# Kernel optimization log

Measured on AMD Instinct MI355X. Metric: run time of the kernel, lower is better.

The kernel has to match this reference:

```python
import jax, jax.numpy as jnp
import numpy as np

B, IN_F, OUT_F, KD = 256, 1024, 128, 16


def setup_inputs() -> dict:
    key = jax.random.key(0)
    k1, k2 = jax.random.split(key)
    x = jax.random.normal(k1, (B, IN_F), dtype=jnp.float32)
    t_mat = jax.random.normal(k2, (IN_F, OUT_F, KD), dtype=jnp.float32)
    return {"x": x, "t_mat": t_mat}


def reference(x, t_mat):
    # Projection: [B, in] @ [in, out*kd] -> [B, out, kd]
    m = jnp.einsum('bi,iok->bok', x, t_mat)
    # All-pairs L1 distance over kernel dim: [B, B, out]
    norm = jnp.sum(jnp.abs(m[:, None, :, :] - m[None, :, :, :]), axis=-1)
    # exp(-norm) summed over the partner axis; subtract 1 for self-pair (norm=0 -> exp=1)
    o_b = jnp.sum(jnp.exp(-norm), axis=1) - 1.0  # [B, out]
    return jnp.concatenate([x, o_b], axis=1)  # [B, in + out]
```

## Files before the change

### kernel.cpp

```cpp
#include <hip/hip_runtime.h>
#include <hip/hip_fp16.h>


#define BATCH 256
#define INF   1024
#define OUTF  128
#define KDIM  16
#define TCOLS 2048
#define OCOLS 1152
#define XB    1032
#define PMW   12

typedef __attribute__((ext_vector_type(8))) short short8;
typedef __attribute__((ext_vector_type(4))) float f32x4;

__device__ inline unsigned pack_bf2(float lo, float hi) {
    return __builtin_amdgcn_perm(__float_as_uint(hi), __float_as_uint(lo), 0x07060302u);
}
__device__ inline unsigned short bf_trunc(float f) {
    return (unsigned short)(__float_as_uint(f) >> 16);
}

__global__ __launch_bounds__(512) void k_prep(const float* __restrict__ x,
                                              unsigned short* __restrict__ xf,
                                              float* __restrict__ out) {
    const int t = blockIdx.x * 512 + threadIdx.x;
    const int mt = t >> 11, ks = (t >> 6) & 31, lane = t & 63;
    const int l15 = lane & 15, q = lane >> 4;

    const float* src = x + (mt * 16 + l15) * INF + ks * 32 + q * 8;
    float4 v0 = *reinterpret_cast<const float4*>(src);
    float4 v1 = *reinterpret_cast<const float4*>(src + 4);
    union { unsigned u[4]; short8 s; } ua;
    ua.u[0] = pack_bf2(v0.x, v0.y);
    ua.u[1] = pack_bf2(v0.z, v0.w);
    ua.u[2] = pack_bf2(v1.x, v1.y);
    ua.u[3] = pack_bf2(v1.z, v1.w);
    reinterpret_cast<short8*>(xf)[t] = ua.s;

    #pragma unroll
    for (int j = t; j < 65536; j += 32768) {
        const int r = j >> 8, c = j & 255;
        reinterpret_cast<float4*>(out)[r * 288 + c] =
            reinterpret_cast<const float4*>(x)[j];
    }
}

__global__ __launch_bounds__(256, 2) void k_gemm(const float* __restrict__ T,
                                                 const unsigned short* __restrict__ xf,
                                                 __half* __restrict__ mh) {
    const int blk = blockIdx.x;
    const int o   = blk & 127;
    const int mq  = blk >> 7;
    const int tid = threadIdx.x;
    const int wave = tid >> 6, lane = tid & 63;
    const int l15 = lane & 15, q = lane >> 4;

    __shared__ unsigned short bs[16][XB];
    __shared__ __half pmout[64][16];

    const int mt = mq * 4 + wave;
    const short8* xr = reinterpret_cast<const short8*>(xf) + mt * 2048 + lane;

    short8 a[32];
    #pragma unroll
    for (int ks = 0; ks < 32; ++ks) a[ks] = xr[ks * 64];
    __builtin_amdgcn_sched_barrier(0);

    {
        const int kb = tid >> 2, n0 = (tid & 3) * 4;
        #pragma unroll
        for (int g = 0; g < 4; ++g) {
            float4 tv[4];
            #pragma unroll
            for (int p = 0; p < 4; ++p)
                tv[p] = *reinterpret_cast<const float4*>(
                    &T[((g * 4 + p) * 64 + kb) * TCOLS + o * KDIM + n0]);
            #pragma unroll
            for (int p = 0; p < 4; ++p) {
                const int k = (g * 4 + p) * 64 + kb;
                bs[n0 + 0][k] = bf_trunc(tv[p].x);
                bs[n0 + 1][k] = bf_trunc(tv[p].y);
                bs[n0 + 2][k] = bf_trunc(tv[p].z);
                bs[n0 + 3][k] = bf_trunc(tv[p].w);
            }
        }
    }
    __syncthreads();

    f32x4 acc = {0.f, 0.f, 0.f, 0.f};
    #pragma unroll
    for (int ks = 0; ks < 32; ++ks) {
        short8 bfr = *reinterpret_cast<const short8*>(&bs[l15][ks * 32 + q * 8]);
        acc = __builtin_amdgcn_mfma_f32_16x16x32_bf16(a[ks], bfr, acc, 0, 0, 0);
    }

    #pragma unroll
    for (int r = 0; r < 4; ++r)
        pmout[wave * 16 + q * 4 + r][l15] = __float2half(acc[r]);
    __syncthreads();

    if (tid < 128) {
        const int row = tid >> 1, hh = tid & 1;
        uint4 v = *reinterpret_cast<const uint4*>(&pmout[row][hh * 8]);
        *reinterpret_cast<uint4*>(&mh[o * (BATCH * KDIM) + (mq * 64 + row) * KDIM + hh * 8]) = v;
    }
}

__global__ __launch_bounds__(1024, 4) void k_pair(const __half* __restrict__ mh,
                                                  float* __restrict__ out) {
    const int blk = blockIdx.x;
    const int o   = blk & 127;
    const int h   = blk >> 7;
    const int tid = threadIdx.x;

    __shared__ __half2 pm[BATCH][PMW];
    __shared__ float part[32][128];

    if (tid < 512) {
        uint4 v = *reinterpret_cast<const uint4*>(
            &mh[o * (BATCH * KDIM) + (tid >> 1) * KDIM + (tid & 1) * 8]);
        *reinterpret_cast<uint4*>(&pm[tid >> 1][(tid & 1) * 4]) = v;
    }
    __syncthreads();

    const int i1 = tid & 31;
    const int bsel = tid >> 5;
    __half2 my[4][8];
    #pragma unroll
    for (int r = 0; r < 4; ++r) {
        union { uint4 u[2]; __half2 hh[8]; } c;
        c.u[0] = *reinterpret_cast<const uint4*>(&pm[h * 128 + r * 32 + i1][0]);
        c.u[1] = *reinterpret_cast<const uint4*>(&pm[h * 128 + r * 32 + i1][4]);
        #pragma unroll
        for (int j = 0; j < 8; ++j) my[r][j] = c.hh[j];
    }

    union U16 { uint4 u[2]; __half2 hh[8]; };
    float tot[4] = {0.f, 0.f, 0.f, 0.f};
    const int b2_lo = bsel * 8;

    U16 c0, c1;
    c0.u[0] = *reinterpret_cast<const uint4*>(&pm[b2_lo][0]);
    c0.u[1] = *reinterpret_cast<const uint4*>(&pm[b2_lo][4]);

    #pragma unroll
    for (int ib = 0; ib < 8; ib += 2) {
        c1.u[0] = *reinterpret_cast<const uint4*>(&pm[b2_lo + ib + 1][0]);
        c1.u[1] = *reinterpret_cast<const uint4*>(&pm[b2_lo + ib + 1][4]);
        #pragma unroll
        for (int r = 0; r < 4; ++r) {
            __half2 e0 = __habs2(__hsub2(my[r][0], c0.hh[0]));
            __half2 e1 = __habs2(__hsub2(my[r][1], c0.hh[1]));
            __half2 e2 = __habs2(__hsub2(my[r][2], c0.hh[2]));
            __half2 e3 = __habs2(__hsub2(my[r][3], c0.hh[3]));
            e0 = __hadd2(e0, __habs2(__hsub2(my[r][4], c0.hh[4])));
            e1 = __hadd2(e1, __habs2(__hsub2(my[r][5], c0.hh[5])));
            e2 = __hadd2(e2, __habs2(__hsub2(my[r][6], c0.hh[6])));
            e3 = __hadd2(e3, __habs2(__hsub2(my[r][7], c0.hh[7])));
            __half2 es = __hadd2(__hadd2(e0, e1), __hadd2(e2, e3));
            float n = __low2float(es) + __high2float(es);
            tot[r] += __expf(-n);
        }
        if (ib + 2 < 8) {
            c0.u[0] = *reinterpret_cast<const uint4*>(&pm[b2_lo + ib + 2][0]);
            c0.u[1] = *reinterpret_cast<const uint4*>(&pm[b2_lo + ib + 2][4]);
        }
        #pragma unroll
        for (int r = 0; r < 4; ++r) {
            __half2 e0 = __habs2(__hsub2(my[r][0], c1.hh[0]));
            __half2 e1 = __habs2(__hsub2(my[r][1], c1.hh[1]));
            __half2 e2 = __habs2(__hsub2(my[r][2], c1.hh[2]));
            __half2 e3 = __habs2(__hsub2(my[r][3], c1.hh[3]));
            e0 = __hadd2(e0, __habs2(__hsub2(my[r][4], c1.hh[4])));
            e1 = __hadd2(e1, __habs2(__hsub2(my[r][5], c1.hh[5])));
            e2 = __hadd2(e2, __habs2(__hsub2(my[r][6], c1.hh[6])));
            e3 = __hadd2(e3, __habs2(__hsub2(my[r][7], c1.hh[7])));
            __half2 es = __hadd2(__hadd2(e0, e1), __hadd2(e2, e3));
            float n = __low2float(es) + __high2float(es);
            tot[r] += __expf(-n);
        }
    }
    #pragma unroll
    for (int r = 0; r < 4; ++r)
        part[bsel][r * 32 + i1] = tot[r];
    __syncthreads();

    {
        const int g = tid >> 7, b1 = tid & 127;
        float s = part[g * 4 + 0][b1] + part[g * 4 + 1][b1]
                + part[g * 4 + 2][b1] + part[g * 4 + 3][b1];
        __syncthreads();
        part[g * 4][b1] = s;
    }
    __syncthreads();
    if (tid < 128) {
        float s = -1.0f;
        #pragma unroll
        for (int g = 0; g < 8; ++g) s += part[g * 4][tid];
        out[(h * 128 + tid) * OCOLS + INF + o] = s;
    }
}

extern "C" void kernel_launch(void* const* d_in, const int* in_sizes, int n_in,
                              void* d_out, int out_size, void* d_ws, size_t ws_size,
                              hipStream_t stream) {
    const float* x = (const float*)d_in[0];
    const float* T = (const float*)d_in[1];
    float* out = (float*)d_out;
    unsigned short* xf = (unsigned short*)d_ws;
    __half* mh = (__half*)((char*)d_ws + (1u << 20));

    k_prep<<<64, 512, 0, stream>>>(x, xf, out);
    k_gemm<<<512, 256, 0, stream>>>(T, xf, mh);
    k_pair<<<256, 1024, 0, stream>>>(mh, out);
}
```

Baseline: 80.02 us.

## Fuse projection GEMM into pairwise kernel, removing intermediate global buffer

Merges the bf16 MFMA projection kernel into the pairwise L1/exp kernel. Each 1024-thread block computes the full 256x16 projection for its output feature directly into shared memory, which removes one launch and the global round trip through the fp16 intermediate. Both blocks with the same output feature (h=0,1) now recompute the same projection, doubling GEMM work and T reads. Register use is kept down by double-buffering A fragments in groups of 8.

```diff
diff --git a/kernel.cpp b/kernel.cpp
--- a/kernel.cpp
+++ b/kernel.cpp
@@ -46,81 +46,79 @@
     }
 }
 
-__global__ __launch_bounds__(256, 2) void k_gemm(const float* __restrict__ T,
-                                                 const unsigned short* __restrict__ xf,
-                                                 __half* __restrict__ mh) {
-    const int blk = blockIdx.x;
-    const int o   = blk & 127;
-    const int mq  = blk >> 7;
-    const int tid = threadIdx.x;
-    const int wave = tid >> 6, lane = tid & 63;
-    const int l15 = lane & 15, q = lane >> 4;
-
-    __shared__ unsigned short bs[16][XB];
-    __shared__ __half pmout[64][16];
-
-    const int mt = mq * 4 + wave;
-    const short8* xr = reinterpret_cast<const short8*>(xf) + mt * 2048 + lane;
-
-    short8 a[32];
-    #pragma unroll
-    for (int ks = 0; ks < 32; ++ks) a[ks] = xr[ks * 64];
-    __builtin_amdgcn_sched_barrier(0);
-
-    {
-        const int kb = tid >> 2, n0 = (tid & 3) * 4;
-        #pragma unroll
-        for (int g = 0; g < 4; ++g) {
-            float4 tv[4];
-            #pragma unroll
-            for (int p = 0; p < 4; ++p)
-                tv[p] = *reinterpret_cast<const float4*>(
-                    &T[((g * 4 + p) * 64 + kb) * TCOLS + o * KDIM + n0]);
-            #pragma unroll
-            for (int p = 0; p < 4; ++p) {
-                const int k = (g * 4 + p) * 64 + kb;
-                bs[n0 + 0][k] = bf_trunc(tv[p].x);
-                bs[n0 + 1][k] = bf_trunc(tv[p].y);
-                bs[n0 + 2][k] = bf_trunc(tv[p].z);
-                bs[n0 + 3][k] = bf_trunc(tv[p].w);
-            }
-        }
-    }
-    __syncthreads();
-
-    f32x4 acc = {0.f, 0.f, 0.f, 0.f};
-    #pragma unroll
-    for (int ks = 0; ks < 32; ++ks) {
-        short8 bfr = *reinterpret_cast<const short8*>(&bs[l15][ks * 32 + q * 8]);
-        acc = __builtin_amdgcn_mfma_f32_16x16x32_bf16(a[ks], bfr, acc, 0, 0, 0);
-    }
-
-    #pragma unroll
-    for (int r = 0; r < 4; ++r)
-        pmout[wave * 16 + q * 4 + r][l15] = __float2half(acc[r]);
-    __syncthreads();
-
-    if (tid < 128) {
-        const int row = tid >> 1, hh = tid & 1;
-        uint4 v = *reinterpret_cast<const uint4*>(&pmout[row][hh * 8]);
-        *reinterpret_cast<uint4*>(&mh[o * (BATCH * KDIM) + (mq * 64 + row) * KDIM + hh * 8]) = v;
-    }
-}
-
-__global__ __launch_bounds__(1024, 4) void k_pair(const __half* __restrict__ mh,
-                                                  float* __restrict__ out) {
+__global__ __launch_bounds__(1024, 4) void k_fused2(const float* __restrict__ T,
+                                                    const unsigned short* __restrict__ xf,
+                                                    float* __restrict__ out) {
     const int blk = blockIdx.x;
     const int o   = blk & 127;
     const int h   = blk >> 7;
     const int tid = threadIdx.x;
-
+    const int wave = tid >> 6, lane = tid & 63;
+    const int l15 = lane & 15, q = lane >> 4;
+
+    __shared__ unsigned short bs[16][XB];
     __shared__ __half2 pm[BATCH][PMW];
     __shared__ float part[32][128];
 
-    if (tid < 512) {
-        uint4 v = *reinterpret_cast<const uint4*>(
-            &mh[o * (BATCH * KDIM) + (tid >> 1) * KDIM + (tid & 1) * 8]);
-        *reinterpret_cast<uint4*>(&pm[tid >> 1][(tid & 1) * 4]) = v;
+    const short8* xr = reinterpret_cast<const short8*>(xf) + wave * 2048 + lane;
+
+    short8 fa[8], fb[8];
+    #pragma unroll
+    for (int f = 0; f < 8; ++f) fa[f] = xr[f * 64];
+    #pragma unroll
+    for (int f = 0; f < 8; ++f) fb[f] = xr[(8 + f) * 64];
+    __builtin_amdgcn_sched_barrier(0);
+
+    {
+        const int kb = tid >> 2, n0 = (tid & 3) * 4;
+        float4 tv[4];
+        #pragma unroll
+        for (int p = 0; p < 4; ++p)
+            tv[p] = *reinterpret_cast<const float4*>(
+                &T[(p * 256 + kb) * TCOLS + o * KDIM + n0]);
+        #pragma unroll
+        for (int p = 0; p < 4; ++p) {
+            const int k = p * 256 + kb;
+            bs[n0 + 0][k] = bf_trunc(tv[p].x);
+            bs[n0 + 1][k] = bf_trunc(tv[p].y);
+            bs[n0 + 2][k] = bf_trunc(tv[p].z);
+            bs[n0 + 3][k] = bf_trunc(tv[p].w);
+        }
+    }
+    __syncthreads();
+
+    f32x4 acc = {0.f, 0.f, 0.f, 0.f};
+    #pragma unroll
+    for (int f = 0; f < 8; ++f) {
+        short8 bfr = *reinterpret_cast<const short8*>(&bs[l15][f * 32 + q * 8]);
+        acc = __builtin_amdgcn_mfma_f32_16x16x32_bf16(fa[f], bfr, acc, 0, 0, 0);
+    }
+    #pragma unroll
+    for (int f = 0; f < 8; ++f) fa[f] = xr[(16 + f) * 64];
+    #pragma unroll
+    for (int f = 0; f < 8; ++f) {
+        short8 bfr = *reinterpret_cast<const short8*>(&bs[l15][(8 + f) * 32 + q * 8]);
+        acc = __builtin_amdgcn_mfma_f32_16x16x32_bf16(fb[f], bfr, acc, 0, 0, 0);
+    }
+    #pragma unroll
+    for (int f = 0; f < 8; ++f) fb[f] = xr[(24 + f) * 64];
+    __builtin_amdgcn_sched_barrier(0);
+    #pragma unroll
+    for (int f = 0; f < 8; ++f) {
+        short8 bfr = *reinterpret_cast<const short8*>(&bs[l15][(16 + f) * 32 + q * 8]);
+        acc = __builtin_amdgcn_mfma_f32_16x16x32_bf16(fa[f], bfr, acc, 0, 0, 0);
+    }
+    #pragma unroll
+    for (int f = 0; f < 8; ++f) {
+        short8 bfr = *reinterpret_cast<const short8*>(&bs[l15][(24 + f) * 32 + q * 8]);
+        acc = __builtin_amdgcn_mfma_f32_16x16x32_bf16(fb[f], bfr, acc, 0, 0, 0);
+    }
+
+    {
+        __half* pmh = reinterpret_cast<__half*>(pm);
+        #pragma unroll
+        for (int r = 0; r < 4; ++r)
+            pmh[(wave * 16 + q * 4 + r) * (2 * PMW) + l15] = __float2half(acc[r]);
     }
     __syncthreads();
 
@@ -209,9 +207,7 @@
     const float* T = (const float*)d_in[1];
     float* out = (float*)d_out;
     unsigned short* xf = (unsigned short*)d_ws;
-    __half* mh = (__half*)((char*)d_ws + (1u << 20));
 
     k_prep<<<64, 512, 0, stream>>>(x, xf, out);
-    k_gemm<<<512, 256, 0, stream>>>(T, xf, mh);
-    k_pair<<<256, 1024, 0, stream>>>(mh, out);
-}
+    k_fused2<<<256, 1024, 0, stream>>>(T, xf, out);
+}
```

Result: no change. 79.19 us (-1.0%).
